# Kernel tuning notes

Measured on AMD Instinct MI355X. Metric: run time of the kernel, lower is better.

The kernel has to match this reference:

```python
import jax, jax.numpy as jnp
import numpy as np

ALPHA = 0.99   # config.alpha_grape
GAMMA = 0.999  # config.gamma
LAMBD = 0.7    # config.lambd_grape
T, A = 262144, 64


def setup_inputs() -> dict:
    key = jax.random.key(0)
    ks = jax.random.split(key, 7)
    q = jax.random.normal(ks[0], (T + 1, A), jnp.float32)
    q_tar = jax.random.normal(ks[1], (T + 1, A), jnp.float32)
    # pi / mu are probability distributions over actions (softmax of logits)
    pi = jax.nn.softmax(jax.random.normal(ks[2], (T + 1, A), jnp.float32), axis=-1)
    mu_t = jax.nn.softmax(jax.random.normal(ks[3], (T, A), jnp.float32), axis=-1)
    a_t = jax.random.randint(ks[4], (T,), 0, A, dtype=jnp.int32)
    r_t = jax.random.normal(ks[5], (T,), jnp.float32)
    done_t = jax.random.randint(ks[6], (T,), 0, 2, dtype=jnp.int32)
    return dict(q=q, q_tar=q_tar, pi=pi, a_t=a_t, r_t=r_t, mu_t=mu_t, done_t=done_t)


def reference(q, q_tar, pi, a_t, r_t, mu_t, done_t):
    # GRAPE.compute_targets
    l = q.shape[0] - 1
    idx = jnp.arange(l)
    pi_t, pi_tp1 = pi[:-1], pi[1:]
    q_t, q_tp1 = q[:-1], q_tar[1:]
    q_t_a = q_t[idx, a_t]                              # [T]
    v_t = jnp.sum(pi_t * q_t, axis=1)                  # [T]
    v_tp1 = jnp.sum(pi_tp1 * q_tp1, axis=1)            # [T]
    done_f = done_t.astype(q.dtype)
    q_t_a_est = r_t + (1.0 - done_f) * GAMMA * v_tp1
    td_error = q_t_a_est - q_t_a
    rho_t_a = pi_t[idx, a_t] / mu_t[idx, a_t]
    c_t_a = LAMBD * jnp.clip(rho_t_a, 0.0, 1.0)

    # backward-in-time first-order recurrence over y'
    def step(y_prime, xs):
        est, td, rho, c, d = xs
        y = jnp.where(d > 0.5, 0.0, y_prime)           # reset at episode end
        g = est + y
        y_new = LAMBD * GAMMA * rho * td + GAMMA * c * y
        return y_new, g

    _, g_q = jax.lax.scan(
        step, jnp.float32(0.0),
        (q_t_a_est, td_error, rho_t_a, c_t_a, done_f),
        reverse=True,
    )
    targets_q = g_q + ALPHA * (q_t_a - v_t)            # [T]
    advantages = (1.0 - ALPHA) * (q_t - v_t[:, None])  # [T, A]
    return targets_q, advantages
```

## Files before the change

kernel.cpp:

```cpp
#include <hip/hip_runtime.h>

#define GAMMA 0.999f
#define LAMBD 0.7f
#define ALPHA 0.99f

constexpr int A_DIM = 64;
constexpr int CH    = 256;

__global__ __launch_bounds__(256, 6)
void k_main(const float* __restrict__ q, const float* __restrict__ q_tar,
            const float* __restrict__ pi, const int* __restrict__ a_t,
            const float* __restrict__ r_t, const float* __restrict__ mu_t,
            const int* __restrict__ done_t,
            float* __restrict__ adv_out,
            float2* __restrict__ comb, float2* __restrict__ cab)
{
    __shared__ float sQa[CH], sRho[CH], sKm[CH], sRt[CH];
    __shared__ float sV[CH], sVp[CH];
    __shared__ float sA[CH], sB[CH];

    const int tid  = threadIdx.x;
    const int wave = tid >> 6, lane = tid & 63;
    const int sub  = lane >> 4, li = lane & 15;
    const int R0   = blockIdx.x * CH;

    {
        int r = R0 + tid;
        int a = a_t[r];
        sRt[tid] = r_t[r];
        sKm[tid] = 1.0f - (float)done_t[r];
        float qa = q[r * A_DIM + a];
        float pa = pi[r * A_DIM + a];
        float ma = mu_t[r * A_DIM + a];
        sQa[tid]  = qa;
        sRho[tid] = pa / ma;
    }

    #pragma unroll 2
    for (int i = 0; i < 8; ++i) {
        int lrowA = wave * 64 + i * 8 + sub;
        int lrowB = lrowA + 4;
        int gA = (R0 + lrowA) * A_DIM + li * 4;
        int gB = (R0 + lrowB) * A_DIM + li * 4;

        float4 piA  = *(const float4*)&pi[gA];
        float4 qA   = *(const float4*)&q[gA];
        float4 pipA = *(const float4*)&pi[gA + A_DIM];
        float4 qpA  = *(const float4*)&q_tar[gA + A_DIM];
        float4 piB  = *(const float4*)&pi[gB];
        float4 qB   = *(const float4*)&q[gB];
        float4 pipB = *(const float4*)&pi[gB + A_DIM];
        float4 qpB  = *(const float4*)&q_tar[gB + A_DIM];

        float s0A = piA.x*qA.x + piA.y*qA.y + piA.z*qA.z + piA.w*qA.w;
        float s1A = pipA.x*qpA.x + pipA.y*qpA.y + pipA.z*qpA.z + pipA.w*qpA.w;
        float s0B = piB.x*qB.x + piB.y*qB.y + piB.z*qB.z + piB.w*qB.w;
        float s1B = pipB.x*qpB.x + pipB.y*qpB.y + pipB.z*qpB.z + pipB.w*qpB.w;
        #pragma unroll
        for (int off = 1; off < 16; off <<= 1) {
            s0A += __shfl_xor(s0A, off);
            s1A += __shfl_xor(s1A, off);
            s0B += __shfl_xor(s0B, off);
            s1B += __shfl_xor(s1B, off);
        }

        float4 advA, advB;
        advA.x = (1.0f - ALPHA) * (qA.x - s0A);
        advA.y = (1.0f - ALPHA) * (qA.y - s0A);
        advA.z = (1.0f - ALPHA) * (qA.z - s0A);
        advA.w = (1.0f - ALPHA) * (qA.w - s0A);
        advB.x = (1.0f - ALPHA) * (qB.x - s0B);
        advB.y = (1.0f - ALPHA) * (qB.y - s0B);
        advB.z = (1.0f - ALPHA) * (qB.z - s0B);
        advB.w = (1.0f - ALPHA) * (qB.w - s0B);
        *(float4*)&adv_out[gA] = advA;
        *(float4*)&adv_out[gB] = advB;

        if (li == 0) {
            sV[lrowA]  = s0A;  sVp[lrowA] = s1A;
            sV[lrowB]  = s0B;  sVp[lrowB] = s1B;
        }
    }
    __syncthreads();

    float s0    = sV[tid],  s1 = sVp[tid];
    float kmask = sKm[tid];
    float qa    = sQa[tid];
    float rho   = sRho[tid];
    float est = sRt[tid] + kmask * (GAMMA * s1);
    float td  = est - qa;
    float c   = LAMBD * fminf(fmaxf(rho, 0.0f), 1.0f);
    float Fa  = (LAMBD * GAMMA) * rho * td;
    float Fb  = kmask * (GAMMA * c);
    float E   = est + ALPHA * (qa - s0);

    float Ai = Fa, Bi = Fb;
    sA[tid] = Ai; sB[tid] = Bi;
    __syncthreads();
    #pragma unroll
    for (int off = 1; off < CH; off <<= 1) {
        float An = 0.0f, Bn = 1.0f;
        if (tid + off < CH) { An = sA[tid + off]; Bn = sB[tid + off]; }
        __syncthreads();
        Ai += Bi * An; Bi *= Bn;
        sA[tid] = Ai; sB[tid] = Bi;
        __syncthreads();
    }
    float Xa = 0.0f, Xb = 1.0f;
    if (tid + 1 < CH) { Xa = sA[tid + 1]; Xb = sB[tid + 1]; }
    comb[R0 + tid] = make_float2(E + kmask * Xa, kmask * Xb);
    if (tid == 0) cab[blockIdx.x] = make_float2(Ai, Bi);
}

__global__ __launch_bounds__(256, 8)
void k_fin(const float2* __restrict__ comb, const float2* __restrict__ cab,
           float* __restrict__ targets, int nch)
{
    __shared__ float sA[256], sB[256];
    __shared__ float sYe;
    const int tid = threadIdx.x, bid = blockIdx.x;

    const float4* cab4 = (const float4*)cab;
    float4 u0 = cab4[2 * tid];
    float4 u1 = cab4[2 * tid + 1];
    float A = u0.x, B = u0.y;
    A += B * u0.z; B *= u0.w;
    A += B * u1.x; B *= u1.y;
    A += B * u1.z; B *= u1.w;
    sA[tid] = A; sB[tid] = B;
    __syncthreads();
    #pragma unroll
    for (int off = 1; off < 256; off <<= 1) {
        float An = 0.0f, Bn = 1.0f;
        if (tid + off < 256) { An = sA[tid + off]; Bn = sB[tid + off]; }
        __syncthreads();
        A += B * An; B *= Bn;
        sA[tid] = A; sB[tid] = B;
        __syncthreads();
    }
    if (tid == 0) {
        int c1 = bid + 1;
        int jq = c1 >> 2, rq = c1 & 3;
        float ye;
        if (rq == 0) {
            ye = (jq < 256) ? sA[jq] : 0.0f;
        } else {
            float Aa = (jq + 1 < 256) ? sA[jq + 1] : 0.0f;
            float Bb = (jq + 1 < 256) ? sB[jq + 1] : 1.0f;
            for (int k2 = 4 * jq + 3; k2 >= c1; --k2) {
                float2 cv = cab[k2];
                Aa = cv.x + cv.y * Aa;
                Bb = cv.y * Bb;
            }
            ye = Aa;
        }
        sYe = ye;
    }
    __syncthreads();

    float2 uw = comb[bid * CH + tid];
    targets[bid * CH + tid] = uw.x + uw.y * sYe;
}

extern "C" void kernel_launch(void* const* d_in, const int* in_sizes, int n_in,
                              void* d_out, int out_size, void* d_ws, size_t ws_size,
                              hipStream_t stream) {
    const float* q      = (const float*)d_in[0];
    const float* q_tar  = (const float*)d_in[1];
    const float* pi     = (const float*)d_in[2];
    const int*   a_t    = (const int*)  d_in[3];
    const float* r_t    = (const float*)d_in[4];
    const float* mu_t   = (const float*)d_in[5];
    const int*   done_t = (const int*)  d_in[6];

    const int T   = in_sizes[3];
    const int nch = T / CH;

    float* targets = (float*)d_out;
    float* adv     = (float*)d_out + T;

    char* ws = (char*)d_ws;
    float2* comb = (float2*)ws;              ws += (size_t)8 * T;
    float2* cab  = (float2*)ws;

    k_main<<<nch, 256, 0, stream>>>(q, q_tar, pi, a_t, r_t, mu_t, done_t,
                                    adv, comb, cab);
    k_fin<<<nch, 256, 0, stream>>>(comb, cab, targets, nch);
}
```

Baseline: 66.13 us.

## Halve chunk size and replace shared-memory scans with wave shuffle scans

Shrinks each block to 128 threads and 128 rows, and replaces the barrier-heavy shared-memory Hillis-Steele scan of the affine recurrence with an intra-wave __shfl_down scan plus a two-wave combine through shared memory. The finalize kernel has each thread fold 16 chunk summaries serially, then runs the same shuffle scan and handles the remainder with a serial walk. The aim is to drop the many __syncthreads and LDS round trips. In exchange it doubles the block count, lengthens the serial per-thread work in k_fin, and raises the serial tail loop to up to 15 steps.

After: 66.52 us. About the same (+0.6%).

```diff
diff --git a/kernel.cpp b/kernel.cpp
--- a/kernel.cpp
+++ b/kernel.cpp
@@ -5,9 +5,10 @@
 #define ALPHA 0.99f
 
 constexpr int A_DIM = 64;
-constexpr int CH    = 256;
-
-__global__ __launch_bounds__(256, 6)
+constexpr int CH    = 128;
+constexpr int BLK   = 128;
+
+__global__ __launch_bounds__(BLK, 8)
 void k_main(const float* __restrict__ q, const float* __restrict__ q_tar,
             const float* __restrict__ pi, const int* __restrict__ a_t,
             const float* __restrict__ r_t, const float* __restrict__ mu_t,
@@ -17,7 +18,7 @@
 {
     __shared__ float sQa[CH], sRho[CH], sKm[CH], sRt[CH];
     __shared__ float sV[CH], sVp[CH];
-    __shared__ float sA[CH], sB[CH];
+    __shared__ float sWA[2], sWB[2];
 
     const int tid  = threadIdx.x;
     const int wave = tid >> 6, lane = tid & 63;
@@ -77,8 +78,8 @@
         *(float4*)&adv_out[gB] = advB;
 
         if (li == 0) {
-            sV[lrowA]  = s0A;  sVp[lrowA] = s1A;
-            sV[lrowB]  = s0B;  sVp[lrowB] = s1B;
+            sV[lrowA] = s0A;  sVp[lrowA] = s1A;
+            sV[lrowB] = s0B;  sVp[lrowB] = s1B;
         }
     }
     __syncthreads();
@@ -95,59 +96,76 @@
     float E   = est + ALPHA * (qa - s0);
 
     float Ai = Fa, Bi = Fb;
-    sA[tid] = Ai; sB[tid] = Bi;
-    __syncthreads();
     #pragma unroll
-    for (int off = 1; off < CH; off <<= 1) {
-        float An = 0.0f, Bn = 1.0f;
-        if (tid + off < CH) { An = sA[tid + off]; Bn = sB[tid + off]; }
-        __syncthreads();
-        Ai += Bi * An; Bi *= Bn;
-        sA[tid] = Ai; sB[tid] = Bi;
-        __syncthreads();
-    }
-    float Xa = 0.0f, Xb = 1.0f;
-    if (tid + 1 < CH) { Xa = sA[tid + 1]; Xb = sB[tid + 1]; }
+    for (int off = 1; off < 64; off <<= 1) {
+        float An = __shfl_down(Ai, off);
+        float Bn = __shfl_down(Bi, off);
+        if (lane + off < 64) { Ai += Bi * An; Bi *= Bn; }
+    }
+    if (lane == 0) { sWA[wave] = Ai; sWB[wave] = Bi; }
+    float Xa = __shfl_down(Ai, 1);
+    float Xb = __shfl_down(Bi, 1);
+    if (lane == 63) { Xa = 0.0f; Xb = 1.0f; }
+    __syncthreads();
+    if (wave == 0) {
+        float W1a = sWA[1], W1b = sWB[1];
+        Xa = Xa + Xb * W1a;
+        Xb = Xb * W1b;
+    }
     comb[R0 + tid] = make_float2(E + kmask * Xa, kmask * Xb);
-    if (tid == 0) cab[blockIdx.x] = make_float2(Ai, Bi);
+    if (tid == 0) {
+        float W1a = sWA[1], W1b = sWB[1];
+        cab[blockIdx.x] = make_float2(Ai + Bi * W1a, Bi * W1b);
+    }
 }
 
-__global__ __launch_bounds__(256, 8)
+__global__ __launch_bounds__(BLK, 8)
 void k_fin(const float2* __restrict__ comb, const float2* __restrict__ cab,
            float* __restrict__ targets, int nch)
 {
-    __shared__ float sA[256], sB[256];
+    __shared__ float sXa[BLK], sXb[BLK];
+    __shared__ float sWA[2], sWB[2];
     __shared__ float sYe;
     const int tid = threadIdx.x, bid = blockIdx.x;
+    const int wave = tid >> 6, lane = tid & 63;
 
     const float4* cab4 = (const float4*)cab;
-    float4 u0 = cab4[2 * tid];
-    float4 u1 = cab4[2 * tid + 1];
-    float A = u0.x, B = u0.y;
-    A += B * u0.z; B *= u0.w;
-    A += B * u1.x; B *= u1.y;
-    A += B * u1.z; B *= u1.w;
-    sA[tid] = A; sB[tid] = B;
-    __syncthreads();
+    float A = 0.0f, B = 1.0f;
     #pragma unroll
-    for (int off = 1; off < 256; off <<= 1) {
-        float An = 0.0f, Bn = 1.0f;
-        if (tid + off < 256) { An = sA[tid + off]; Bn = sB[tid + off]; }
-        __syncthreads();
-        A += B * An; B *= Bn;
-        sA[tid] = A; sB[tid] = B;
-        __syncthreads();
-    }
+    for (int j = 0; j < 8; ++j) {
+        float4 u = cab4[tid * 8 + j];
+        A += B * u.x; B *= u.y;
+        A += B * u.z; B *= u.w;
+    }
+
+    float Ai = A, Bi = B;
+    #pragma unroll
+    for (int off = 1; off < 64; off <<= 1) {
+        float An = __shfl_down(Ai, off);
+        float Bn = __shfl_down(Bi, off);
+        if (lane + off < 64) { Ai += Bi * An; Bi *= Bn; }
+    }
+    if (lane == 0) { sWA[wave] = Ai; sWB[wave] = Bi; }
+    float Xa = __shfl_down(Ai, 1);
+    float Xb = __shfl_down(Bi, 1);
+    if (lane == 63) { Xa = 0.0f; Xb = 1.0f; }
+    __syncthreads();
+    if (wave == 0) {
+        Xa = Xa + Xb * sWA[1];
+        Xb = Xb * sWB[1];
+    }
+    sXa[tid] = Xa; sXb[tid] = Xb;
+    __syncthreads();
+
     if (tid == 0) {
         int c1 = bid + 1;
-        int jq = c1 >> 2, rq = c1 & 3;
         float ye;
-        if (rq == 0) {
-            ye = (jq < 256) ? sA[jq] : 0.0f;
+        if (c1 >= nch) {
+            ye = 0.0f;
         } else {
-            float Aa = (jq + 1 < 256) ? sA[jq + 1] : 0.0f;
-            float Bb = (jq + 1 < 256) ? sB[jq + 1] : 1.0f;
-            for (int k2 = 4 * jq + 3; k2 >= c1; --k2) {
+            int jq = c1 >> 4, rq = c1 & 15;
+            float Aa = sXa[jq], Bb = sXb[jq];
+            for (int k2 = 16 * jq + 15; k2 >= c1; --k2) {
                 float2 cv = cab[k2];
                 Aa = cv.x + cv.y * Aa;
                 Bb = cv.y * Bb;
@@ -183,7 +201,7 @@
     float2* comb = (float2*)ws;              ws += (size_t)8 * T;
     float2* cab  = (float2*)ws;
 
-    k_main<<<nch, 256, 0, stream>>>(q, q_tar, pi, a_t, r_t, mu_t, done_t,
+    k_main<<<nch, BLK, 0, stream>>>(q, q_tar, pi, a_t, r_t, mu_t, done_t,
                                     adv, comb, cab);
-    k_fin<<<nch, 256, 0, stream>>>(comb, cab, targets, nch);
+    k_fin<<<nch, BLK, 0, stream>>>(comb, cab, targets, nch);
 }
```
